# Kernel optimization log

Hardware: AMD Instinct MI355X
Metric: run time of the kernel (lower is better)

The kernel has to match this reference:

```python
import jax, jax.numpy as jnp
import numpy as np

B, T, G, M, D = 8, 2048, 2, 1024, 256
ALPHA = -1.0      # config['dist_to_logits_alpha']
TAU = 2.0         # curr_temp = max_temp at init
EPS = 1e-10


def setup_inputs() -> dict:
    key = jax.random.key(0)
    k1, k2, k3 = jax.random.split(key, 3)
    x = jax.random.normal(k1, (B, T, G * D), dtype=jnp.float32)
    # nn.init.uniform_(embedding, -0.999, 0.999)
    embedding = jax.random.uniform(k2, (G, M, D), dtype=jnp.float32, minval=-0.999, maxval=0.999)
    # uniform noise for gumbel sampling, clipped away from {0,1}
    gumbel_u = jax.random.uniform(k3, (B * T, G, M), dtype=jnp.float32, minval=1e-6, maxval=1.0 - 1e-6)
    return {"x": x, "embedding": embedding, "gumbel_u": gumbel_u}


def reference(x, embedding, gumbel_u):
    b, t, c = x.shape
    g, m, d = embedding.shape
    xf = x.reshape(-1, g, d)                                  # [N, G, D]

    sq_e = jnp.sum(embedding ** 2, axis=-1)                   # [G, M]
    sq_x = jnp.sum(xf ** 2, axis=-1, keepdims=True)           # [N, G, 1]
    cross = jnp.einsum('ngd,gmd->ngm', xf, embedding)         # [N, G, M]
    logits = ALPHA * (sq_e[None] + sq_x - 2.0 * cross)        # [N, G, M]

    # hard-assignment code perplexity
    hard_x = jax.nn.one_hot(jnp.argmax(logits, axis=-1), m, dtype=logits.dtype)
    hard_probs = hard_x.mean(axis=0)                          # [G, M]
    code_perplexity = -jnp.sum(hard_probs * jnp.log2(hard_probs + EPS), axis=-1)

    # soft-assignment prob perplexity
    avg_probs = jax.nn.softmax(logits, axis=-1).mean(axis=0)  # [G, M]
    prob_perplexity = -jnp.sum(avg_probs * jnp.log2(avg_probs + EPS), axis=-1)

    # gumbel-softmax (hard=True, straight-through)
    gumbels = -jnp.log(-jnp.log(gumbel_u))
    y_soft = jax.nn.softmax((logits + gumbels) / TAU, axis=-1)
    idx = jnp.argmax(y_soft, axis=-1)                         # [N, G]
    y_hard = jax.nn.one_hot(idx, m, dtype=y_soft.dtype)
    st = y_hard + y_soft - jax.lax.stop_gradient(y_soft)      # straight-through one-hot

    # weighted sum over the codebook (avoids [N, G, M, D] blowup of the original)
    quantized = jnp.einsum('ngm,gmd->ngd', st, embedding).reshape(b, t, c)

    quantization_inds = idx.reshape(b, t, g).astype(jnp.int32)
    # use_vq_loss=True: F.mse_loss(x, quantized.detach())
    commitment_loss = jnp.mean((x - jax.lax.stop_gradient(quantized)) ** 2)

    return quantized, code_perplexity, prob_perplexity, quantization_inds, commitment_loss
```

## Files before the change

### kernel.cpp

```cpp
#include <hip/hip_runtime.h>
#include <math.h>

#define NTOT 16384
#define GG 2
#define MM 1024
#define DD 256

#define OFF_Q  ((size_t)0)
#define OFF_CP ((size_t)8388608)
#define OFF_PP ((size_t)8388610)
#define OFF_I  ((size_t)8388612)
#define OFF_L  ((size_t)8421380)

#define SHIFT 40.0f
#define REFINE_GAP 0.03f

typedef __attribute__((ext_vector_type(8))) short bf16x8;
typedef __attribute__((ext_vector_type(4))) float f32x4;
typedef unsigned short u16;
typedef unsigned int u32;

__device__ inline float wave_sum_f(float v) {
#pragma unroll
  for (int o = 32; o > 0; o >>= 1) v += __shfl_xor(v, o);
  return v;
}
__device__ inline u16 f2bf(float f) {
  u32 u = __float_as_uint(f);
  return (u16)((u + 0x7fffu + ((u >> 16) & 1u)) >> 16);
}
__device__ inline float bf2f(u16 h) {
  return __uint_as_float(((u32)h) << 16);
}
__device__ inline void async16(const void* g, void* l) {
  __builtin_amdgcn_global_load_lds(
      (const __attribute__((address_space(1))) u32*)g,
      (__attribute__((address_space(3))) u32*)l, 16, 0, 0);
}

#define WS_INVZ   32768
#define WS_EHSW   163840
#define WS_ELSW   1212416
#define WS_EST    2260992
#define WS_NEED3  (2260992ull + 2ull * MM * (size_t)NTOT * GG)

__global__ void vq_init2(const float* __restrict__ emb, float* __restrict__ sq_e,
                         float* __restrict__ avg, int* __restrict__ hist,
                         double* __restrict__ loss, u16* __restrict__ eh,
                         u16* __restrict__ el, int do_split) {
  const int row = blockIdx.x * 4 + (threadIdx.x >> 6);
  const int lane = threadIdx.x & 63;
  float4 e4 = *(const float4*)&emb[(size_t)row * DD + lane * 4];
  float s = e4.x * e4.x + e4.y * e4.y + e4.z * e4.z + e4.w * e4.w;
  s = wave_sum_f(s);
  if (do_split) {
    ushort4 h, l;
    h.x = f2bf(e4.x); l.x = f2bf(e4.x - bf2f(h.x));
    h.y = f2bf(e4.y); l.y = f2bf(e4.y - bf2f(h.y));
    h.z = f2bf(e4.z); l.z = f2bf(e4.z - bf2f(h.z));
    h.w = f2bf(e4.w); l.w = f2bf(e4.w - bf2f(h.w));
    *(ushort4*)&eh[(size_t)row * DD + lane * 4] = h;
    *(ushort4*)&el[(size_t)row * DD + lane * 4] = l;
  }
  if (lane == 0) sq_e[row] = s;
  if (blockIdx.x == 0) {
    for (int i = threadIdx.x; i < GG * MM; i += 256) { avg[i] = 0.f; hist[i] = 0; }
    if (threadIdx.x == 0) *loss = 0.0;
  }
}

__global__ void vq_init_swz(const float* __restrict__ emb, u16* __restrict__ eh_sw,
                            u16* __restrict__ el_sw) {
  int tid = blockIdx.x * 256 + threadIdx.x;
  int g = tid >> 15, rem = tid & 32767;
  int col = rem >> 5, kc = rem & 31;
  const float* src = emb + ((size_t)(g * MM + col)) * DD + kc * 8;
  float4 fa = *(const float4*)src;
  float4 fb = *(const float4*)(src + 4);
  float f[8] = {fa.x, fa.y, fa.z, fa.w, fb.x, fb.y, fb.z, fb.w};
  u16 hi[8], lo[8];
#pragma unroll
  for (int j = 0; j < 8; ++j) {
    hi[j] = f2bf(f[j]);
    lo[j] = f2bf(f[j] - bf2f(hi[j]));
  }
  int ct = col >> 6, cg = (col >> 4) & 3, l15 = col & 15;
  int ks = kc >> 2, quad = kc & 3;
  size_t chunk = ((((size_t)g * 16 + ct) * 8 + ks) * 4 + cg) * 64 + quad * 16 + l15;
  ushort4* dh = (ushort4*)(eh_sw + chunk * 8);
  ushort4* dl = (ushort4*)(el_sw + chunk * 8);
  dh[0] = make_ushort4(hi[0], hi[1], hi[2], hi[3]);
  dh[1] = make_ushort4(hi[4], hi[5], hi[6], hi[7]);
  dl[0] = make_ushort4(lo[0], lo[1], lo[2], lo[3]);
  dl[1] = make_ushort4(lo[4], lo[5], lo[6], lo[7]);
}

__global__ __launch_bounds__(512, 2) void vq_main3(
    const float* __restrict__ x, const float* __restrict__ emb,
    const float* __restrict__ gum, const float* __restrict__ sq_e,
    const u16* __restrict__ eh_sw, const u16* __restrict__ el_sw,
    float* __restrict__ out, u16* __restrict__ est, float* __restrict__ invZ_ws,
    int* __restrict__ hist, double* __restrict__ loss) {
  __shared__ u16 bt[2][32768];
  __shared__ int fidx_lds[128];

  const int g = blockIdx.y;
  const int n0 = blockIdx.x * 128;
  const int t = threadIdx.x;
  const int wave = t >> 6, lane = t & 63;
  const int quad = lane >> 4, l15 = lane & 15;
  const int nw = n0 + wave * 16;

  float* xs = (float*)&bt[0][0];
  {
    const float* xb = x + (size_t)nw * (GG * DD) + (size_t)g * DD;
#pragma unroll 4
    for (int j = 0; j < 16; ++j) {
      float4 v = *(const float4*)(xb + (size_t)j * (GG * DD) + lane * 4);
      *(float4*)&xs[wave * 4096 + j * 256 + ((lane ^ (j & 7)) << 2)] = v;
    }
  }

  bf16x8 ah[8], al[8];
#pragma unroll
  for (int ks = 0; ks < 8; ++ks) {
    int row = l15;
    int c0 = ks * 8 + quad * 2;
    const float* base = &xs[wave * 4096 + row * 256];
    float4 f0 = *(const float4*)&base[((c0 ^ (row & 7)) << 2)];
    float4 f1 = *(const float4*)&base[(((c0 + 1) ^ (row & 7)) << 2)];
    float f[8] = {f0.x, f0.y, f0.z, f0.w, f1.x, f1.y, f1.z, f1.w};
#pragma unroll
    for (int j = 0; j < 8; ++j) {
      u16 h = f2bf(f[j]);
      ah[ks][j] = (short)h;
      al[ks][j] = (short)f2bf(f[j] - bf2f(h));
    }
  }
  __syncthreads();

  const u16* sgh = eh_sw + (size_t)g * 16 * 16384;
  const u16* sgl = el_sw + (size_t)g * 16 * 16384;

  auto stage = [&](int ct, int buf) {
    const u16* sh = sgh + (size_t)ct * 16384;
    const u16* sl = sgl + (size_t)ct * 16384;
    u16* dh = &bt[buf][0];
    u16* dl = &bt[buf][16384];
#pragma unroll
    for (int j = 0; j < 4; ++j) {
      int slot = j * 8 + wave;
      async16(sh + slot * 512 + lane * 8, dh + slot * 512);
      async16(sl + slot * 512 + lane * 8, dl + slot * 512);
    }
  };

  float Zl[4], hv[4], z1[4], z2[4];
  int hid[4], i1[4], i2[4];
#pragma unroll
  for (int i = 0; i < 4; ++i) {
    Zl[i] = 0.f; hv[i] = -INFINITY; z1[i] = -INFINITY; z2[i] = -INFINITY;
    hid[i] = 0; i1[i] = 0; i2[i] = 0;
  }

  stage(0, 0);

#pragma unroll 1
  for (int ct = 0; ct < 16; ++ct) {
    __syncthreads();
    if (ct < 15) stage(ct + 1, (ct + 1) & 1);
    const u16* bh_p = &bt[ct & 1][0];
    const u16* bl_p = &bt[ct & 1][16384];
#pragma unroll 1
    for (int cg = 0; cg < 4; ++cg) {
      const int colG = ct * 64 + cg * 16 + l15;
      float sqv = sq_e[g * MM + colG];
      float gv[4];
#pragma unroll
      for (int r = 0; r < 4; ++r)
        gv[r] = gum[((size_t)(nw + quad * 4 + r) * GG + g) * MM + colG];

      f32x4 c0 = {0,0,0,0}, c1 = {0,0,0,0}, c2 = {0,0,0,0};
#pragma unroll
      for (int ks = 0; ks < 8; ++ks) {
        int off = ((ks * 4 + cg) * 64 + lane) * 8;
        bf16x8 bh = *(const bf16x8*)(bh_p + off);
        bf16x8 bl = *(const bf16x8*)(bl_p + off);
        c0 = __builtin_amdgcn_mfma_f32_16x16x32_bf16(ah[ks], bh, c0, 0, 0, 0);
        c1 = __builtin_amdgcn_mfma_f32_16x16x32_bf16(ah[ks], bl, c1, 0, 0, 0);
        c2 = __builtin_amdgcn_mfma_f32_16x16x32_bf16(al[ks], bh, c2, 0, 0, 0);
      }
      ushort4 pk;
      u16* pp = (u16*)&pk;
#pragma unroll
      for (int r = 0; r < 4; ++r) {
        float lp = 2.f * (c0[r] + c1[r] + c2[r]) - sqv + SHIFT;
        float ev = expf(fminf(lp, 80.f));
        Zl[r] += ev;
        pp[r] = f2bf(ev);
        if (lp > hv[r]) { hv[r] = lp; hid[r] = colG; }
        float zz = lp - logf(-logf(gv[r]));
        if (zz > z1[r]) {
          z2[r] = z1[r]; i2[r] = i1[r];
          z1[r] = zz; i1[r] = colG;
        } else if (zz > z2[r]) {
          z2[r] = zz; i2[r] = colG;
        }
      }
      *(ushort4*)&est[((size_t)(g * MM + colG) << 14) + nw + quad * 4] = pk;
    }
  }

#pragma unroll 1
  for (int r = 0; r < 4; ++r) {
    const int row = wave * 16 + quad * 4 + r;
    const int n = n0 + row;
    float Zr = Zl[r], hvr = hv[r];
    int hir = hid[r];
    float v1 = z1[r], v2 = z2[r];
    int j1 = i1[r], j2 = i2[r];
#pragma unroll
    for (int o = 1; o <= 8; o <<= 1) {
      Zr += __shfl_xor(Zr, o);
      float ohv = __shfl_xor(hvr, o); int ohi = __shfl_xor(hir, o);
      if (ohv > hvr || (ohv == hvr && ohi < hir)) { hvr = ohv; hir = ohi; }
      float w1 = __shfl_xor(v1, o), w2 = __shfl_xor(v2, o);
      int k1 = __shfl_xor(j1, o), k2 = __shfl_xor(j2, o);
      if (w1 > v1 || (w1 == v1 && k1 < j1)) {
        if (v1 > w2 || (v1 == w2 && j1 < k2)) { v2 = v1; j2 = j1; }
        else { v2 = w2; j2 = k2; }
        v1 = w1; j1 = k1;
      } else if (w1 > v2 || (w1 == v2 && k1 < j2)) { v2 = w1; j2 = k1; }
    }
    int fidx = j1;
    if (v1 - v2 < REFINE_GAP) {
      const float* xrow = x + (size_t)n * (GG * DD) + (size_t)g * DD;
      const float* eA = emb + ((size_t)g * MM + j1) * DD;
      const float* eB = emb + ((size_t)g * MM + j2) * DD;
      double dA = 0, sA = 0, dB = 0, sB = 0;
#pragma unroll
      for (int k = 0; k < 16; ++k) {
        int d = l15 * 16 + k;
        double xv = (double)xrow[d];
        double ea = (double)eA[d], eb = (double)eB[d];
        dA += xv * ea; sA += ea * ea;
        dB += xv * eb; sB += eb * eb;
      }
#pragma unroll
      for (int o = 1; o <= 8; o <<= 1) {
        dA += __shfl_xor(dA, o); sA += __shfl_xor(sA, o);
        dB += __shfl_xor(dB, o); sB += __shfl_xor(sB, o);
      }
      double uA = (double)gum[((size_t)n * GG + g) * MM + j1];
      double uB = (double)gum[((size_t)n * GG + g) * MM + j2];
      double zA = 2.0 * dA - sA - log(-log(uA));
      double zB = 2.0 * dB - sB - log(-log(uB));
      if (zB > zA || (zB == zA && j2 < j1)) fidx = j2;
    }
    if (l15 == 0) {
      out[OFF_I + (size_t)n * GG + g] = (float)fidx;
      atomicAdd(&hist[g * MM + hir], 1);
      invZ_ws[g * NTOT + n] = 1.f / Zr;
      fidx_lds[row] = fidx;
    }
  }
  __syncthreads();

  {
    float ls = 0.f;
#pragma unroll 4
    for (int j = 0; j < 16; ++j) {
      int idx = j * 512 + t;
      int row = idx >> 6, f4 = idx & 63;
      int n = n0 + row, fi = fidx_lds[row];
      float4 e4 = *(const float4*)&emb[((size_t)g * MM + fi) * DD + f4 * 4];
      float4 x4 = *(const float4*)&x[(size_t)n * (GG * DD) + (size_t)g * DD + f4 * 4];
      *(float4*)&out[OFF_Q + (size_t)n * (GG * DD) + (size_t)g * DD + f4 * 4] = e4;
      float dx = x4.x - e4.x, dy = x4.y - e4.y, dz = x4.z - e4.z, dw = x4.w - e4.w;
      ls += dx * dx + dy * dy + dz * dz + dw * dw;
    }
    ls = wave_sum_f(ls);
    if (lane == 0) atomicAdd(loss, (double)ls);
  }
}

__global__ void vq_avg(const u16* __restrict__ est, const float* __restrict__ invZ,
                       float* __restrict__ avg) {
  int wid = blockIdx.x * 4 + (threadIdx.x >> 6);
  int lane = threadIdx.x & 63;
  const u16* base = est + ((size_t)wid << 14);
  const float* zp = invZ + ((wid >> 10) << 14);
  float acc = 0.f;
#pragma unroll 4
  for (int it = 0; it < 64; ++it) {
    int n = it * 256 + lane * 4;
    ushort4 e4 = *(const ushort4*)(base + n);
    float4 z4 = *(const float4*)(zp + n);
    acc += bf2f(e4.x) * z4.x + bf2f(e4.y) * z4.y +
           bf2f(e4.z) * z4.z + bf2f(e4.w) * z4.w;
  }
  acc = wave_sum_f(acc);
  if (lane == 0) avg[wid] = acc;
}

__global__ void vq_fin(const float* __restrict__ avg, const int* __restrict__ hist,
                       const double* __restrict__ loss, float* __restrict__ out) {
  int g = blockIdx.x, t = threadIdx.x;
  float cp = 0.f, pp = 0.f;
  for (int m = t; m < MM; m += 256) {
    float hp = (float)hist[g * MM + m] * (1.f / 16384.f);
    cp += hp * log2f(hp + 1e-10f);
    float ap = avg[g * MM + m] * (1.f / 16384.f);
    pp += ap * log2f(ap + 1e-10f);
  }
  cp = wave_sum_f(cp);
  pp = wave_sum_f(pp);
  __shared__ float sc[4], sp[4];
  int wave = t >> 6, lane = t & 63;
  if (lane == 0) { sc[wave] = cp; sp[wave] = pp; }
  __syncthreads();
  if (t == 0) {
    out[OFF_CP + g] = -(sc[0] + sc[1] + sc[2] + sc[3]);
    out[OFF_PP + g] = -(sp[0] + sp[1] + sp[2] + sp[3]);
    if (g == 0) out[OFF_L] = (float)(*loss * (1.0 / 8388608.0));
  }
}

__global__ __launch_bounds__(256, 3) void vq_main_fast(
    const float* __restrict__ x, const float* __restrict__ emb,
    const float* __restrict__ gum, const float* __restrict__ sq_e,
    const u16* __restrict__ eh, const u16* __restrict__ el,
    float* __restrict__ out, float* __restrict__ avg,
    int* __restrict__ hist, double* __restrict__ loss) {
  __shared__ u16 est_lds[4][16][264];
  __shared__ float colsum[MM];
  __shared__ float red[16][4][8];
  __shared__ float fin_invZ[16];
  __shared__ int fin_idx[16];

  const int g = blockIdx.y;
  const int n0 = blockIdx.x * 16;
  const int t = threadIdx.x;
  const int wave = t >> 6, lane = t & 63;
  const int quad = lane >> 4, l15 = lane & 15;
  const int wm0 = wave * 256;

  for (int i = t; i < MM; i += 256) colsum[i] = 0.f;

  bf16x8 ah[8], al[8];
  {
    const float* xr = x + (size_t)(n0 + l15) * (GG * DD) + (size_t)g * DD + quad * 8;
#pragma unroll
    for (int ks = 0; ks < 8; ++ks) {
      float4 fa = *(const float4*)(xr + ks * 32);
      float4 fb = *(const float4*)(xr + ks * 32 + 4);
      float f[8] = {fa.x, fa.y, fa.z, fa.w, fb.x, fb.y, fb.z, fb.w};
#pragma unroll
      for (int j = 0; j < 8; ++j) {
        u16 h = f2bf(f[j]);
        ah[ks][j] = (short)h;
        al[ks][j] = (short)f2bf(f[j] - bf2f(h));
      }
    }
  }
  const u16* ehb = eh + ((size_t)g * MM + wm0 + l15) * DD + quad * 8;
  const u16* elb = el + ((size_t)g * MM + wm0 + l15) * DD + quad * 8;
  const float* sqb = sq_e + g * MM + wm0 + l15;

  float Z[4] = {0.f, 0.f, 0.f, 0.f};
  float hv[4] = {-INFINITY, -INFINITY, -INFINITY, -INFINITY};
  int hid[4] = {0, 0, 0, 0};
  float z1[4] = {-INFINITY, -INFINITY, -INFINITY, -INFINITY};
  float z2[4] = {-INFINITY, -INFINITY, -INFINITY, -INFINITY};
  int i1[4] = {0, 0, 0, 0}, i2[4] = {0, 0, 0, 0};

#pragma unroll 2
  for (int tt = 0; tt < 16; ++tt) {
    float sqv = sqb[tt * 16];
    float gv[4];
#pragma unroll
    for (int r = 0; r < 4; ++r)
      gv[r] = gum[((size_t)(n0 + quad * 4 + r) * GG + g) * MM + wm0 + tt * 16 + l15];
    f32x4 a0 = {0,0,0,0}, a1 = {0,0,0,0}, a2 = {0,0,0,0};
#pragma unroll
    for (int ks = 0; ks < 8; ++ks) {
      bf16x8 bh = *(const bf16x8*)(ehb + (size_t)tt * 16 * DD + ks * 32);
      bf16x8 bl = *(const bf16x8*)(elb + (size_t)tt * 16 * DD + ks * 32);
      a0 = __builtin_amdgcn_mfma_f32_16x16x32_bf16(ah[ks], bh, a0, 0, 0, 0);
      a1 = __builtin_amdgcn_mfma_f32_16x16x32_bf16(ah[ks], bl, a1, 0, 0, 0);
      a2 = __builtin_amdgcn_mfma_f32_16x16x32_bf16(al[ks], bh, a2, 0, 0, 0);
    }
    const int colL = tt * 16 + l15;
    const int colG = wm0 + colL;
#pragma unroll
    for (int r = 0; r < 4; ++r) {
      float lp = 2.f * (a0[r] + a1[r] + a2[r]) - sqv + SHIFT;
      float ev = expf(fminf(lp, 80.f));
      Z[r] += ev;
      est_lds[wave][quad * 4 + r][colL] = f2bf(ev);
      if (lp > hv[r]) { hv[r] = lp; hid[r] = colG; }
      float zz = lp - logf(-logf(gv[r]));
      if (zz > z1[r]) { z2[r] = z1[r]; i2[r] = i1[r]; z1[r] = zz; i1[r] = colG; }
      else if (zz > z2[r]) { z2[r] = zz; i2[r] = colG; }
    }
  }
#pragma unroll
  for (int r = 0; r < 4; ++r) {
    float Zr = Z[r], hvr = hv[r];
    int hir = hid[r];
    float v1 = z1[r], v2 = z2[r];
    int j1 = i1[r], j2 = i2[r];
#pragma unroll
    for (int o = 1; o <= 8; o <<= 1) {
      Zr += __shfl_xor(Zr, o);
      float ohv = __shfl_xor(hvr, o); int ohi = __shfl_xor(hir, o);
      if (ohv > hvr || (ohv == hvr && ohi < hir)) { hvr = ohv; hir = ohi; }
      float w1 = __shfl_xor(v1, o), w2 = __shfl_xor(v2, o);
      int k1 = __shfl_xor(j1, o), k2 = __shfl_xor(j2, o);
      if (w1 > v1 || (w1 == v1 && k1 < j1)) {
        if (v1 > w2 || (v1 == w2 && j1 < k2)) { v2 = v1; j2 = j1; }
        else { v2 = w2; j2 = k2; }
        v1 = w1; j1 = k1;
      } else if (w1 > v2 || (w1 == v2 && k1 < j2)) { v2 = w1; j2 = k1; }
    }
    if (l15 == 0) {
      float* rp = red[quad * 4 + r][wave];
      rp[0] = Zr; rp[1] = hvr; rp[2] = __int_as_float(hir);
      rp[3] = v1; rp[4] = __int_as_float(j1);
      rp[5] = v2; rp[6] = __int_as_float(j2);
    }
  }
  __syncthreads();
  if (t < 16) {
    const int row = t, n = n0 + row;
    float Zf = 0.f, hvf = -INFINITY; int hif = 0;
    float v1 = -INFINITY, v2 = -INFINITY; int j1 = 0, j2 = 0;
    for (int w = 0; w < 4; ++w) {
      const float* rp = red[row][w];
      Zf += rp[0];
      float ohv = rp[1]; int ohi = __float_as_int(rp[2]);
      if (ohv > hvf || (ohv == hvf && ohi < hif)) { hvf = ohv; hif = ohi; }
      float w1 = rp[3], w2 = rp[5];
      int k1 = __float_as_int(rp[4]), k2 = __float_as_int(rp[6]);
      if (w1 > v1 || (w1 == v1 && k1 < j1)) {
        if (v1 > w2 || (v1 == w2 && j1 < k2)) { v2 = v1; j2 = j1; }
        else { v2 = w2; j2 = k2; }
        v1 = w1; j1 = k1;
      } else if (w1 > v2 || (w1 == v2 && k1 < j2)) { v2 = w1; j2 = k1; }
    }
    int fidx = j1;
    if (v1 - v2 < REFINE_GAP) {
      const float* xrow = x + (size_t)n * (GG * DD) + (size_t)g * DD;
      const float* eA = emb + ((size_t)g * MM + j1) * DD;
      const float* eB = emb + ((size_t)g * MM + j2) * DD;
      double dA = 0, sA = 0, dB = 0, sB = 0;
      for (int d = 0; d < DD; ++d) {
        double xv = xrow[d], ea = eA[d], eb = eB[d];
        dA += xv * ea; sA += ea * ea;
        dB += xv * eb; sB += eb * eb;
      }
      double uA = gum[((size_t)n * GG + g) * MM + j1];
      double uB = gum[((size_t)n * GG + g) * MM + j2];
      double zA = 2.0 * dA - sA - log(-log(uA));
      double zB = 2.0 * dB - sB - log(-log(uB));
      if (zB > zA || (zB == zA && j2 < j1)) fidx = j2;
    }
    out[OFF_I + (size_t)n * GG + g] = (float)fidx;
    atomicAdd(&hist[g * MM + hif], 1);
    fin_invZ[row] = 1.f / Zf;
    fin_idx[row] = fidx;
  }
  __syncthreads();
  {
    const int row = t >> 4, c = (t & 15) * 16;
    const int n = n0 + row, fidx = fin_idx[row];
    const float* er = emb + ((size_t)g * MM + fidx) * DD + c;
    const float* xq = x + (size_t)n * (GG * DD) + (size_t)g * DD + c;
    float* op = out + OFF_Q + (size_t)n * (GG * DD) + (size_t)g * DD + c;
    float ls = 0.f;
#pragma unroll
    for (int j = 0; j < 4; ++j) {
      float4 e4 = *(const float4*)(er + j * 4);
      float4 x4 = *(const float4*)(xq + j * 4);
      *(float4*)(op + j * 4) = e4;
      float dx = x4.x - e4.x, dy = x4.y - e4.y, dz = x4.z - e4.z, dw = x4.w - e4.w;
      ls += dx * dx + dy * dy + dz * dz + dw * dw;
    }
    ls = wave_sum_f(ls);
    if (lane == 0) atomicAdd(loss, (double)ls);
  }
  float iZ[4];
#pragma unroll
  for (int r = 0; r < 4; ++r) iZ[r] = fin_invZ[quad * 4 + r];
#pragma unroll 1
  for (int tt = 0; tt < 16; ++tt) {
    float v = 0.f;
#pragma unroll
    for (int r = 0; r < 4; ++r)
      v += bf2f(est_lds[wave][quad * 4 + r][tt * 16 + l15]) * iZ[r];
    v += __shfl_xor(v, 16);
    v += __shfl_xor(v, 32);
    if (lane < 16) colsum[wm0 + tt * 16 + lane] += v;
  }
  __syncthreads();
  for (int i = t; i < MM; i += 256) atomicAdd(&avg[g * MM + i], colsum[i]);
}

extern "C" void kernel_launch(void* const* d_in, const int* in_sizes, int n_in,
                              void* d_out, int out_size, void* d_ws, size_t ws_size,
                              hipStream_t stream) {
  const float* x = (const float*)d_in[0];
  const float* emb = (const float*)d_in[1];
  const float* gum = (const float*)d_in[2];
  float* out = (float*)d_out;

  float* sq_e = (float*)d_ws;
  float* avg = (float*)((char*)d_ws + 8192);
  int* hist = (int*)((char*)d_ws + 16384);
  double* loss = (double*)((char*)d_ws + 24576);

  if (ws_size >= WS_NEED3) {
    float* invZ = (float*)((char*)d_ws + WS_INVZ);
    u16* eh_sw = (u16*)((char*)d_ws + WS_EHSW);
    u16* el_sw = (u16*)((char*)d_ws + WS_ELSW);
    u16* est = (u16*)((char*)d_ws + WS_EST);
    vq_init2<<<512, 256, 0, stream>>>(emb, sq_e, avg, hist, loss, eh_sw, el_sw, 0);
    vq_init_swz<<<256, 256, 0, stream>>>(emb, eh_sw, el_sw);
    vq_main3<<<dim3(NTOT / 128, GG), 512, 0, stream>>>(
        x, emb, gum, sq_e, eh_sw, el_sw, out, est, invZ, hist, loss);
    vq_avg<<<512, 256, 0, stream>>>(est, invZ, avg);
    vq_fin<<<GG, 256, 0, stream>>>(avg, hist, loss, out);
  } else {
    u16* eh = (u16*)((char*)d_ws + 32768);
    u16* el = eh + (size_t)GG * MM * DD;
    vq_init2<<<512, 256, 0, stream>>>(emb, sq_e, avg, hist, loss, eh, el, 1);
    vq_main_fast<<<dim3(NTOT / 16, GG), 256, 0, stream>>>(
        x, emb, gum, sq_e, eh, el, out, avg, hist, loss);
    vq_fin<<<GG, 256, 0, stream>>>(avg, hist, loss, out);
  }
}
```

Baseline: 364.3 us.

## Halve rows per block, split codebook columns across wave pairs with LDS merge

The main kernel now handles 64 rows per block instead of 128, and each row-slab is processed by two waves that each take half of every 32-column codebook tile. Their softmax sums, argmax and top-2 Gumbel candidates are merged through shared memory. LDS per block is halved and launch bounds are raised to 4 blocks per CU, for more occupancy and twice as many blocks. The change also swaps expf/logf for fast intrinsics plus a series approximation of -log(u) near 1. This adds a barrier and merge step and slightly changes the numerics of the Gumbel argmax, which the refine path partly covers.

```diff
diff --git a/kernel.cpp b/kernel.cpp
--- a/kernel.cpp
+++ b/kernel.cpp
@@ -36,6 +36,12 @@
   __builtin_amdgcn_global_load_lds(
       (const __attribute__((address_space(1))) u32*)g,
       (__attribute__((address_space(3))) u32*)l, 16, 0, 0);
+}
+__device__ inline float neg_log_acc(float u) {
+  float t1 = 1.0f - u;
+  float se = t1 * (1.f + t1 * (0.5f + t1 * (0.33333334f + t1 * 0.25f)));
+  float fl = -__logf(u);
+  return (t1 < 0.015625f) ? se : fl;
 }
 
 #define WS_INVZ   32768
@@ -95,46 +101,51 @@
   dl[1] = make_ushort4(lo[4], lo[5], lo[6], lo[7]);
 }
 
-__global__ __launch_bounds__(512, 2) void vq_main3(
+__global__ __launch_bounds__(512, 4) void vq_main3(
     const float* __restrict__ x, const float* __restrict__ emb,
     const float* __restrict__ gum, const float* __restrict__ sq_e,
     const u16* __restrict__ eh_sw, const u16* __restrict__ el_sw,
     float* __restrict__ out, u16* __restrict__ est, float* __restrict__ invZ_ws,
     int* __restrict__ hist, double* __restrict__ loss) {
-  __shared__ u16 bt[2][32768];
-  __shared__ int fidx_lds[128];
+  __shared__ u16 bt[2][16384];
+  __shared__ float mrg[64][8];
+  __shared__ int fidx_lds[64];
 
   const int g = blockIdx.y;
-  const int n0 = blockIdx.x * 128;
+  const int n0 = blockIdx.x * 64;
   const int t = threadIdx.x;
   const int wave = t >> 6, lane = t & 63;
+  const int s = wave & 3, h = wave >> 2;
   const int quad = lane >> 4, l15 = lane & 15;
-  const int nw = n0 + wave * 16;
+  const int nw = n0 + s * 16;
 
   float* xs = (float*)&bt[0][0];
   {
-    const float* xb = x + (size_t)nw * (GG * DD) + (size_t)g * DD;
-#pragma unroll 4
-    for (int j = 0; j < 16; ++j) {
-      float4 v = *(const float4*)(xb + (size_t)j * (GG * DD) + lane * 4);
-      *(float4*)&xs[wave * 4096 + j * 256 + ((lane ^ (j & 7)) << 2)] = v;
-    }
-  }
+    const float* xb = x + (size_t)n0 * (GG * DD) + (size_t)g * DD;
+#pragma unroll
+    for (int j = 0; j < 8; ++j) {
+      int idx = j * 512 + t;
+      int row = idx >> 6, ch = idx & 63;
+      float4 v = *(const float4*)(xb + (size_t)row * (GG * DD) + ch * 4);
+      *(float4*)&xs[row * 256 + ((ch ^ (row & 7)) << 2)] = v;
+    }
+  }
+  __syncthreads();
 
   bf16x8 ah[8], al[8];
 #pragma unroll
   for (int ks = 0; ks < 8; ++ks) {
-    int row = l15;
+    int row = s * 16 + l15;
     int c0 = ks * 8 + quad * 2;
-    const float* base = &xs[wave * 4096 + row * 256];
+    const float* base = &xs[row * 256];
     float4 f0 = *(const float4*)&base[((c0 ^ (row & 7)) << 2)];
     float4 f1 = *(const float4*)&base[(((c0 + 1) ^ (row & 7)) << 2)];
     float f[8] = {f0.x, f0.y, f0.z, f0.w, f1.x, f1.y, f1.z, f1.w};
 #pragma unroll
     for (int j = 0; j < 8; ++j) {
-      u16 h = f2bf(f[j]);
-      ah[ks][j] = (short)h;
-      al[ks][j] = (short)f2bf(f[j] - bf2f(h));
+      u16 hh = f2bf(f[j]);
+      ah[ks][j] = (short)hh;
+      al[ks][j] = (short)f2bf(f[j] - bf2f(hh));
     }
   }
   __syncthreads();
@@ -142,16 +153,19 @@
   const u16* sgh = eh_sw + (size_t)g * 16 * 16384;
   const u16* sgl = el_sw + (size_t)g * 16 * 16384;
 
-  auto stage = [&](int ct, int buf) {
+  auto stage = [&](int t32, int buf) {
+    int ct = t32 >> 1, pb = (t32 & 1) * 2;
     const u16* sh = sgh + (size_t)ct * 16384;
     const u16* sl = sgl + (size_t)ct * 16384;
     u16* dh = &bt[buf][0];
-    u16* dl = &bt[buf][16384];
-#pragma unroll
-    for (int j = 0; j < 4; ++j) {
+    u16* dl = &bt[buf][8192];
+#pragma unroll
+    for (int j = 0; j < 2; ++j) {
       int slot = j * 8 + wave;
-      async16(sh + slot * 512 + lane * 8, dh + slot * 512);
-      async16(sl + slot * 512 + lane * 8, dl + slot * 512);
+      int ks = slot >> 1, cg2 = slot & 1;
+      int so = (ks * 4 + pb + cg2) * 512;
+      async16(sh + so + lane * 8, dh + slot * 512);
+      async16(sl + so + lane * 8, dl + slot * 512);
     }
   };
 
@@ -166,55 +180,52 @@
   stage(0, 0);
 
 #pragma unroll 1
-  for (int ct = 0; ct < 16; ++ct) {
+  for (int t32 = 0; t32 < 32; ++t32) {
     __syncthreads();
-    if (ct < 15) stage(ct + 1, (ct + 1) & 1);
-    const u16* bh_p = &bt[ct & 1][0];
-    const u16* bl_p = &bt[ct & 1][16384];
-#pragma unroll 1
-    for (int cg = 0; cg < 4; ++cg) {
-      const int colG = ct * 64 + cg * 16 + l15;
-      float sqv = sq_e[g * MM + colG];
-      float gv[4];
-#pragma unroll
-      for (int r = 0; r < 4; ++r)
-        gv[r] = gum[((size_t)(nw + quad * 4 + r) * GG + g) * MM + colG];
-
-      f32x4 c0 = {0,0,0,0}, c1 = {0,0,0,0}, c2 = {0,0,0,0};
-#pragma unroll
-      for (int ks = 0; ks < 8; ++ks) {
-        int off = ((ks * 4 + cg) * 64 + lane) * 8;
-        bf16x8 bh = *(const bf16x8*)(bh_p + off);
-        bf16x8 bl = *(const bf16x8*)(bl_p + off);
-        c0 = __builtin_amdgcn_mfma_f32_16x16x32_bf16(ah[ks], bh, c0, 0, 0, 0);
-        c1 = __builtin_amdgcn_mfma_f32_16x16x32_bf16(ah[ks], bl, c1, 0, 0, 0);
-        c2 = __builtin_amdgcn_mfma_f32_16x16x32_bf16(al[ks], bh, c2, 0, 0, 0);
+    if (t32 < 31) stage(t32 + 1, (t32 + 1) & 1);
+    const u16* bh_p = &bt[t32 & 1][0];
+    const u16* bl_p = &bt[t32 & 1][8192];
+    const int colG = t32 * 32 + h * 16 + l15;
+    float sqv = sq_e[g * MM + colG];
+    float gv[4];
+#pragma unroll
+    for (int r = 0; r < 4; ++r)
+      gv[r] = gum[((size_t)(nw + quad * 4 + r) * GG + g) * MM + colG];
+
+    f32x4 c0 = {0,0,0,0}, c1 = {0,0,0,0}, c2 = {0,0,0,0};
+#pragma unroll
+    for (int ks = 0; ks < 8; ++ks) {
+      int off = ((ks * 2 + h) * 64 + lane) * 8;
+      bf16x8 bh = *(const bf16x8*)(bh_p + off);
+      bf16x8 bl = *(const bf16x8*)(bl_p + off);
+      c0 = __builtin_amdgcn_mfma_f32_16x16x32_bf16(ah[ks], bh, c0, 0, 0, 0);
+      c1 = __builtin_amdgcn_mfma_f32_16x16x32_bf16(ah[ks], bl, c1, 0, 0, 0);
+      c2 = __builtin_amdgcn_mfma_f32_16x16x32_bf16(al[ks], bh, c2, 0, 0, 0);
+    }
+    ushort4 pk;
+    u16* pp = (u16*)&pk;
+#pragma unroll
+    for (int r = 0; r < 4; ++r) {
+      float lp = 2.f * (c0[r] + c1[r] + c2[r]) - sqv + SHIFT;
+      float ev = __expf(fminf(lp, 80.f));
+      Zl[r] += ev;
+      pp[r] = f2bf(ev);
+      if (lp > hv[r]) { hv[r] = lp; hid[r] = colG; }
+      float zz = lp - __logf(neg_log_acc(gv[r]));
+      if (zz > z1[r]) {
+        z2[r] = z1[r]; i2[r] = i1[r];
+        z1[r] = zz; i1[r] = colG;
+      } else if (zz > z2[r]) {
+        z2[r] = zz; i2[r] = colG;
       }
-      ushort4 pk;
-      u16* pp = (u16*)&pk;
-#pragma unroll
-      for (int r = 0; r < 4; ++r) {
-        float lp = 2.f * (c0[r] + c1[r] + c2[r]) - sqv + SHIFT;
-        float ev = expf(fminf(lp, 80.f));
-        Zl[r] += ev;
-        pp[r] = f2bf(ev);
-        if (lp > hv[r]) { hv[r] = lp; hid[r] = colG; }
-        float zz = lp - logf(-logf(gv[r]));
-        if (zz > z1[r]) {
-          z2[r] = z1[r]; i2[r] = i1[r];
-          z1[r] = zz; i1[r] = colG;
-        } else if (zz > z2[r]) {
-          z2[r] = zz; i2[r] = colG;
-        }
-      }
-      *(ushort4*)&est[((size_t)(g * MM + colG) << 14) + nw + quad * 4] = pk;
-    }
-  }
-
+    }
+    *(ushort4*)&est[((size_t)(g * MM + colG) << 14) + nw + quad * 4] = pk;
+  }
+
+  float Zr4[4], hv4[4], v14[4], v24[4];
+  int hi4[4], j14[4], j24[4];
 #pragma unroll 1
   for (int r = 0; r < 4; ++r) {
-    const int row = wave * 16 + quad * 4 + r;
-    const int n = n0 + row;
     float Zr = Zl[r], hvr = hv[r];
     int hir = hid[r];
     float v1 = z1[r], v2 = z2[r];
@@ -232,44 +243,78 @@
         v1 = w1; j1 = k1;
       } else if (w1 > v2 || (w1 == v2 && k1 < j2)) { v2 = w1; j2 = k1; }
     }
-    int fidx = j1;
-    if (v1 - v2 < REFINE_GAP) {
-      const float* xrow = x + (size_t)n * (GG * DD) + (size_t)g * DD;
-      const float* eA = emb + ((size_t)g * MM + j1) * DD;
-      const float* eB = emb + ((size_t)g * MM + j2) * DD;
-      double dA = 0, sA = 0, dB = 0, sB = 0;
-#pragma unroll
-      for (int k = 0; k < 16; ++k) {
-        int d = l15 * 16 + k;
-        double xv = (double)xrow[d];
-        double ea = (double)eA[d], eb = (double)eB[d];
-        dA += xv * ea; sA += ea * ea;
-        dB += xv * eb; sB += eb * eb;
+    Zr4[r] = Zr; hv4[r] = hvr; hi4[r] = hir;
+    v14[r] = v1; j14[r] = j1; v24[r] = v2; j24[r] = j2;
+    if (h == 1 && l15 == 0) {
+      float* rp = mrg[s * 16 + quad * 4 + r];
+      rp[0] = Zr; rp[1] = hvr; rp[2] = __int_as_float(hir);
+      rp[3] = v1; rp[4] = __int_as_float(j1);
+      rp[5] = v2; rp[6] = __int_as_float(j2);
+    }
+  }
+  __syncthreads();
+
+  if (h == 0) {
+#pragma unroll 1
+    for (int r = 0; r < 4; ++r) {
+      const int row = s * 16 + quad * 4 + r;
+      const int n = n0 + row;
+      float Zr = Zr4[r], hvr = hv4[r];
+      int hir = hi4[r];
+      float v1 = v14[r], v2 = v24[r];
+      int j1 = j14[r], j2 = j24[r];
+      const float* rp = mrg[row];
+      Zr += rp[0];
+      {
+        float ohv = rp[1]; int ohi = __float_as_int(rp[2]);
+        if (ohv > hvr || (ohv == hvr && ohi < hir)) { hvr = ohv; hir = ohi; }
+        float w1 = rp[3], w2 = rp[5];
+        int k1 = __float_as_int(rp[4]), k2 = __float_as_int(rp[6]);
+        if (w1 > v1 || (w1 == v1 && k1 < j1)) {
+          if (v1 > w2 || (v1 == w2 && j1 < k2)) { v2 = v1; j2 = j1; }
+          else { v2 = w2; j2 = k2; }
+          v1 = w1; j1 = k1;
+        } else if (w1 > v2 || (w1 == v2 && k1 < j2)) { v2 = w1; j2 = k1; }
       }
-#pragma unroll
-      for (int o = 1; o <= 8; o <<= 1) {
-        dA += __shfl_xor(dA, o); sA += __shfl_xor(sA, o);
-        dB += __shfl_xor(dB, o); sB += __shfl_xor(sB, o);
+      int fidx = j1;
+      if (v1 - v2 < REFINE_GAP) {
+        const float* xrow = x + (size_t)n * (GG * DD) + (size_t)g * DD;
+        const float* eA = emb + ((size_t)g * MM + j1) * DD;
+        const float* eB = emb + ((size_t)g * MM + j2) * DD;
+        double dA = 0, sA = 0, dB = 0, sB = 0;
+#pragma unroll
+        for (int k = 0; k < 16; ++k) {
+          int d = l15 * 16 + k;
+          double xv = (double)xrow[d];
+          double ea = (double)eA[d], eb = (double)eB[d];
+          dA += xv * ea; sA += ea * ea;
+          dB += xv * eb; sB += eb * eb;
+        }
+#pragma unroll
+        for (int o = 1; o <= 8; o <<= 1) {
+          dA += __shfl_xor(dA, o); sA += __shfl_xor(sA, o);
+          dB += __shfl_xor(dB, o); sB += __shfl_xor(sB, o);
+        }
+        double uA = (double)gum[((size_t)n * GG + g) * MM + j1];
+        double uB = (double)gum[((size_t)n * GG + g) * MM + j2];
+        double zA = 2.0 * dA - sA - log(-log(uA));
+        double zB = 2.0 * dB - sB - log(-log(uB));
+        if (zB > zA || (zB == zA && j2 < j1)) fidx = j2;
       }
-      double uA = (double)gum[((size_t)n * GG + g) * MM + j1];
-      double uB = (double)gum[((size_t)n * GG + g) * MM + j2];
-      double zA = 2.0 * dA - sA - log(-log(uA));
-      double zB = 2.0 * dB - sB - log(-log(uB));
-      if (zB > zA || (zB == zA && j2 < j1)) fidx = j2;
-    }
-    if (l15 == 0) {
-      out[OFF_I + (size_t)n * GG + g] = (float)fidx;
-      atomicAdd(&hist[g * MM + hir], 1);
-      invZ_ws[g * NTOT + n] = 1.f / Zr;
-      fidx_lds[row] = fidx;
+      if (l15 == 0) {
+        out[OFF_I + (size_t)n * GG + g] = (float)fidx;
+        atomicAdd(&hist[g * MM + hir], 1);
+        invZ_ws[g * NTOT + n] = 1.f / Zr;
+        fidx_lds[row] = fidx;
+      }
     }
   }
   __syncthreads();
 
   {
     float ls = 0.f;
-#pragma unroll 4
-    for (int j = 0; j < 16; ++j) {
+#pragma unroll
+    for (int j = 0; j < 8; ++j) {
       int idx = j * 512 + t;
       int row = idx >> 6, f4 = idx & 63;
       int n = n0 + row, fi = fidx_lds[row];
@@ -526,7 +571,7 @@
     u16* est = (u16*)((char*)d_ws + WS_EST);
     vq_init2<<<512, 256, 0, stream>>>(emb, sq_e, avg, hist, loss, eh_sw, el_sw, 0);
     vq_init_swz<<<256, 256, 0, stream>>>(emb, eh_sw, el_sw);
-    vq_main3<<<dim3(NTOT / 128, GG), 512, 0, stream>>>(
+    vq_main3<<<dim3(NTOT / 64, GG), 512, 0, stream>>>(
         x, emb, gum, sq_e, eh_sw, el_sw, out, est, invZ, hist, loss);
     vq_avg<<<512, 256, 0, stream>>>(est, invZ, avg);
     vq_fin<<<GG, 256, 0, stream>>>(avg, hist, loss, out);
```

New measurement: 429.5 us. 17.9% more time.

## Halve LDS tile to raise occupancy and use fast exp/log intrinsics

Applied to the files above, without the earlier changes.

Halves the shared-memory double buffer by staging 32-column half-tiles instead of 64-column tiles. Launch bounds change from 2 to 4 blocks per CU to raise occupancy. The x fragments are now loaded straight from global memory into registers, dropping the LDS staging pass and one barrier, and the first codebook stage is issued before that load so the two overlap. expf/logf become __expf/__logf, with a series expansion guarding -log(u) near 1, and the loss loop is fully unrolled. The risks are register spills under the tighter launch bound, twice as many barriers per codebook pass, and fast-math precision changes that could flip near-tie argmax decisions.

```diff
diff --git a/kernel.cpp b/kernel.cpp
--- a/kernel.cpp
+++ b/kernel.cpp
@@ -36,6 +36,12 @@
   __builtin_amdgcn_global_load_lds(
       (const __attribute__((address_space(1))) u32*)g,
       (__attribute__((address_space(3))) u32*)l, 16, 0, 0);
+}
+__device__ inline float neg_log_acc(float u) {
+  float t1 = 1.0f - u;
+  float se = t1 * (1.f + t1 * (0.5f + t1 * (0.33333334f + t1 * 0.25f)));
+  float fl = -__logf(u);
+  return (t1 < 0.015625f) ? se : fl;
 }
 
 #define WS_INVZ   32768
@@ -95,13 +101,13 @@
   dl[1] = make_ushort4(lo[4], lo[5], lo[6], lo[7]);
 }
 
-__global__ __launch_bounds__(512, 2) void vq_main3(
+__global__ __launch_bounds__(512, 4) void vq_main3(
     const float* __restrict__ x, const float* __restrict__ emb,
     const float* __restrict__ gum, const float* __restrict__ sq_e,
     const u16* __restrict__ eh_sw, const u16* __restrict__ el_sw,
     float* __restrict__ out, u16* __restrict__ est, float* __restrict__ invZ_ws,
     int* __restrict__ hist, double* __restrict__ loss) {
-  __shared__ u16 bt[2][32768];
+  __shared__ u16 bt[2][16384];
   __shared__ int fidx_lds[128];
 
   const int g = blockIdx.y;
@@ -111,49 +117,43 @@
   const int quad = lane >> 4, l15 = lane & 15;
   const int nw = n0 + wave * 16;
 
-  float* xs = (float*)&bt[0][0];
-  {
-    const float* xb = x + (size_t)nw * (GG * DD) + (size_t)g * DD;
-#pragma unroll 4
-    for (int j = 0; j < 16; ++j) {
-      float4 v = *(const float4*)(xb + (size_t)j * (GG * DD) + lane * 4);
-      *(float4*)&xs[wave * 4096 + j * 256 + ((lane ^ (j & 7)) << 2)] = v;
-    }
-  }
-
-  bf16x8 ah[8], al[8];
-#pragma unroll
-  for (int ks = 0; ks < 8; ++ks) {
-    int row = l15;
-    int c0 = ks * 8 + quad * 2;
-    const float* base = &xs[wave * 4096 + row * 256];
-    float4 f0 = *(const float4*)&base[((c0 ^ (row & 7)) << 2)];
-    float4 f1 = *(const float4*)&base[(((c0 + 1) ^ (row & 7)) << 2)];
-    float f[8] = {f0.x, f0.y, f0.z, f0.w, f1.x, f1.y, f1.z, f1.w};
-#pragma unroll
-    for (int j = 0; j < 8; ++j) {
-      u16 h = f2bf(f[j]);
-      ah[ks][j] = (short)h;
-      al[ks][j] = (short)f2bf(f[j] - bf2f(h));
-    }
-  }
-  __syncthreads();
-
   const u16* sgh = eh_sw + (size_t)g * 16 * 16384;
   const u16* sgl = el_sw + (size_t)g * 16 * 16384;
 
-  auto stage = [&](int ct, int buf) {
+  auto stage = [&](int t32, int buf) {
+    int ct = t32 >> 1, pb = (t32 & 1) * 2;
     const u16* sh = sgh + (size_t)ct * 16384;
     const u16* sl = sgl + (size_t)ct * 16384;
     u16* dh = &bt[buf][0];
-    u16* dl = &bt[buf][16384];
-#pragma unroll
-    for (int j = 0; j < 4; ++j) {
+    u16* dl = &bt[buf][8192];
+#pragma unroll
+    for (int j = 0; j < 2; ++j) {
       int slot = j * 8 + wave;
-      async16(sh + slot * 512 + lane * 8, dh + slot * 512);
-      async16(sl + slot * 512 + lane * 8, dl + slot * 512);
+      int ks = slot >> 1, cgp = slot & 1;
+      int so = (ks * 4 + pb + cgp) * 512;
+      async16(sh + so + lane * 8, dh + slot * 512);
+      async16(sl + so + lane * 8, dl + slot * 512);
     }
   };
+
+  stage(0, 0);
+
+  bf16x8 ah[8], al[8];
+  {
+    const float* xr = x + (size_t)(nw + l15) * (GG * DD) + (size_t)g * DD + quad * 8;
+#pragma unroll
+    for (int ks = 0; ks < 8; ++ks) {
+      float4 fa = *(const float4*)(xr + ks * 32);
+      float4 fb = *(const float4*)(xr + ks * 32 + 4);
+      float f[8] = {fa.x, fa.y, fa.z, fa.w, fb.x, fb.y, fb.z, fb.w};
+#pragma unroll
+      for (int j = 0; j < 8; ++j) {
+        u16 h = f2bf(f[j]);
+        ah[ks][j] = (short)h;
+        al[ks][j] = (short)f2bf(f[j] - bf2f(h));
+      }
+    }
+  }
 
   float Zl[4], hv[4], z1[4], z2[4];
   int hid[4], i1[4], i2[4];
@@ -163,17 +163,15 @@
     hid[i] = 0; i1[i] = 0; i2[i] = 0;
   }
 
-  stage(0, 0);
-
 #pragma unroll 1
-  for (int ct = 0; ct < 16; ++ct) {
+  for (int t32 = 0; t32 < 32; ++t32) {
     __syncthreads();
-    if (ct < 15) stage(ct + 1, (ct + 1) & 1);
-    const u16* bh_p = &bt[ct & 1][0];
-    const u16* bl_p = &bt[ct & 1][16384];
+    if (t32 < 31) stage(t32 + 1, (t32 + 1) & 1);
+    const u16* bh_p = &bt[t32 & 1][0];
+    const u16* bl_p = &bt[t32 & 1][8192];
 #pragma unroll 1
-    for (int cg = 0; cg < 4; ++cg) {
-      const int colG = ct * 64 + cg * 16 + l15;
+    for (int cg = 0; cg < 2; ++cg) {
+      const int colG = t32 * 32 + cg * 16 + l15;
       float sqv = sq_e[g * MM + colG];
       float gv[4];
 #pragma unroll
@@ -183,7 +181,7 @@
       f32x4 c0 = {0,0,0,0}, c1 = {0,0,0,0}, c2 = {0,0,0,0};
 #pragma unroll
       for (int ks = 0; ks < 8; ++ks) {
-        int off = ((ks * 4 + cg) * 64 + lane) * 8;
+        int off = ((ks * 2 + cg) * 64 + lane) * 8;
         bf16x8 bh = *(const bf16x8*)(bh_p + off);
         bf16x8 bl = *(const bf16x8*)(bl_p + off);
         c0 = __builtin_amdgcn_mfma_f32_16x16x32_bf16(ah[ks], bh, c0, 0, 0, 0);
@@ -195,11 +193,11 @@
 #pragma unroll
       for (int r = 0; r < 4; ++r) {
         float lp = 2.f * (c0[r] + c1[r] + c2[r]) - sqv + SHIFT;
-        float ev = expf(fminf(lp, 80.f));
+        float ev = __expf(fminf(lp, 80.f));
         Zl[r] += ev;
         pp[r] = f2bf(ev);
         if (lp > hv[r]) { hv[r] = lp; hid[r] = colG; }
-        float zz = lp - logf(-logf(gv[r]));
+        float zz = lp - __logf(neg_log_acc(gv[r]));
         if (zz > z1[r]) {
           z2[r] = z1[r]; i2[r] = i1[r];
           z1[r] = zz; i1[r] = colG;
@@ -268,7 +266,7 @@
 
   {
     float ls = 0.f;
-#pragma unroll 4
+#pragma unroll
     for (int j = 0; j < 16; ++j) {
       int idx = j * 512 + t;
       int row = idx >> 6, f4 = idx & 63;
```

Result: slower. 488.1 us (+34.0%).
